# Kernel tuning notes

Measured on AMD Instinct MI355X. Metric: run time of the kernel, lower is better.

## Reference

```python
import jax, jax.numpy as jnp
import numpy as np

B, N, FREQS, DATA_DIM, WIDTH = 8192, 256, 9, 28, 128
PE_DIM = FREQS * 3 * 2  # 54


def setup_inputs() -> dict:
    rng = np.random.default_rng(0)
    mask = rng.random((B, N)) < 0.5  # ragged per-ray intersection mask
    P = int(mask.sum())             # total packed samples (~1.05M)
    key = jax.random.key(0)
    ks = jax.random.split(key, 6)
    rays_d = jax.random.normal(ks[0], (B, 3), dtype=jnp.float32)
    # sorted intersection distances along each ray (cumsum of positive steps)
    steps = jax.random.uniform(ks[1], (B, N + 1), minval=0.005, maxval=0.03)
    intrs = 2.0 + jnp.cumsum(steps, axis=1)
    data = 0.1 * jax.random.normal(ks[2], (P, DATA_DIM), dtype=jnp.float32)
    in_dim = DATA_DIM + PE_DIM
    W1 = (jax.random.normal(ks[3], (WIDTH, in_dim)) / np.sqrt(in_dim)).astype(jnp.float32)
    b1 = jnp.zeros((WIDTH,), jnp.float32)
    W2 = (jax.random.normal(ks[4], (4, WIDTH)) / np.sqrt(WIDTH)).astype(jnp.float32)
    b2 = jnp.zeros((4,), jnp.float32)
    return {"rays_d": rays_d, "intrs": intrs, "intrs_mask": jnp.asarray(mask),
            "data": data, "W1": W1, "b1": b1, "W2": W2, "b2": b2}


def pos_encode(x, freqs):
    bands = 2.0 ** jnp.arange(freqs, dtype=x.dtype)          # [F]
    xb = x[:, None, :] * bands[None, :, None]                 # [P, F, 3]
    enc = jnp.concatenate([jnp.sin(xb), jnp.cos(xb)], -1)     # [P, F, 6]
    return enc.reshape(x.shape[0], -1)                        # [P, 6F]


def _forward(rays_d, intrs, data, W1, b1, W2, b2, intrs_mask):
    Bn, Np1 = intrs.shape
    Nn = Np1 - 1
    P = data.shape[0]
    # packed row-major positions of valid samples (matches masked_scatter_ order)
    idx = jnp.flatnonzero(intrs_mask, size=P)
    ray_id = idx // Nn                       # repeat_interleave(rays_d, mask.sum(1))
    dir_pe = pos_encode(rays_d[ray_id], FREQS)
    mlp_in = jnp.concatenate([data, dir_pe], axis=-1)   # [P, data_dim + 6F]
    h = jax.nn.relu(mlp_in @ W1.T + b1)
    preact = h @ W2.T + b2                   # [P, 4]
    density_m = jax.nn.relu(preact[:, 0])
    color_m = preact[:, 1:]
    # scatter packed values back to dense [B, N] ray grid
    density = jnp.zeros((Bn * Nn,), preact.dtype).at[idx].set(density_m).reshape(Bn, Nn)
    # sigma2alpha: alpha compositing along each ray
    dists = (intrs[:, 1:] - intrs[:, :-1]) * jnp.linalg.norm(rays_d, axis=-1, keepdims=True)
    alpha = 1.0 - jnp.exp(-density * dists)
    trans = jnp.cumprod(1.0 - alpha + 1e-10, axis=-1)
    cum_light = jnp.concatenate([jnp.ones((Bn, 1), alpha.dtype), trans[:, :-1]], axis=-1)
    abs_light = alpha * cum_light            # per-sample compositing weights
    # shrgb2rgb: weighted color accumulation + white background
    color = jnp.zeros((Bn * Nn, 3), preact.dtype).at[idx].set(color_m).reshape(Bn, Nn, 3)
    rgb = jax.nn.sigmoid(color)
    comp = jnp.sum(abs_light[..., None] * rgb, axis=1)
    comp = comp + (1.0 - jnp.sum(abs_light, axis=-1))[:, None]
    return comp, alpha


def reference(rays_d, intrs, intrs_mask, data, W1, b1, W2, b2):
    return _forward(rays_d, intrs, data, W1, b1, W2, b2, intrs_mask)
```

## Files before the change

### kernel.cpp

```cpp
#include <hip/hip_runtime.h>
#include <hip/hip_bf16.h>
#include <math.h>

#define FREQS 9
#define DATA_DIM 28
#define WIDTH 128
#define IN_DIM 82
#define HST2 72
#define PEST 56

typedef float f32x4 __attribute__((ext_vector_type(4)));
typedef short s16x8 __attribute__((ext_vector_type(8)));

__device__ __forceinline__ short f2bf(float f) {
    unsigned u = __builtin_bit_cast(unsigned, f);
    u += 0x7fffu + ((u >> 16) & 1u);
    return (short)(u >> 16);
}

__device__ __forceinline__ unsigned pk2(float a, float b) {
    float2 t; t.x = a; t.y = b;
    __hip_bfloat162 h = __float22bfloat162_rn(t);
    unsigned r;
    __builtin_memcpy(&r, &h, sizeof(r));
    return r;
}

__device__ __forceinline__ float bf2f(unsigned u16v) {
    unsigned u = u16v << 16;
    return __builtin_bit_cast(float, u);
}

__device__ __forceinline__ void gload_lds16(const void* g, void* l) {
    __builtin_amdgcn_global_load_lds(
        (const __attribute__((address_space(1))) unsigned int*)g,
        (__attribute__((address_space(3))) unsigned int*)l, 16, 0, 0);
}

__device__ __forceinline__ int detect_bytemask(const unsigned* __restrict__ mw, int lane) {
    unsigned w = mw[lane & 63];
    unsigned long long hi = __ballot((w & 0xFFFFFF00u) != 0);
    return hi != 0ull;
}


__global__ __launch_bounds__(256) void k_prep(
    const float* __restrict__ rays_d, const float* __restrict__ W1,
    const float* __restrict__ b1, const float* __restrict__ W2,
    const void* __restrict__ maskp,
    short* __restrict__ W1bf, short* __restrict__ W2bf, float* __restrict__ hpe,
    int* __restrict__ cnt, int Bn, int N)
{
    int tid = threadIdx.x;
    int wid = tid >> 6, lane = tid & 63;

    if (blockIdx.x >= 256) {
        int b = (blockIdx.x - 256) * 4 + wid;
        if (b >= Bn) return;
        const unsigned char* m8 = (const unsigned char*)maskp;
        const int* m32 = (const int*)maskp;
        int fl = detect_bytemask((const unsigned*)maskp, lane);
        int base = 0;
        for (int t = 0; t < N / 64; ++t) {
            int n = t * 64 + lane;
            int mv = fl ? (int)m8[(size_t)b * N + n] : m32[(size_t)b * N + n];
            unsigned long long bal = __ballot(mv != 0);
            base += __popcll(bal);
        }
        if (lane == 0) cnt[b] = base;
        return;
    }

    __shared__ __align__(16) float w1pe[WIDTH * PEST];
    __shared__ __align__(16) float pe_s[4][PEST];

    if (blockIdx.x == 0) {
        for (int t = tid; t < WIDTH * 32; t += 256) {
            int n = t / 32, k = t - n * 32;
            W1bf[t] = (k < DATA_DIM) ? f2bf(W1[n * IN_DIM + k]) : (short)0;
        }
        for (int t = tid; t < 5 * WIDTH; t += 256) {
            int r = t >> 7, k = t & 127;
            W2bf[t] = (r < 4) ? f2bf(W2[r * WIDTH + k]) : (short)0;
        }
    }
    for (int t = tid; t < WIDTH * PEST; t += 256) {
        int row = t / PEST, j = t - row * PEST;
        w1pe[t] = (j < 54) ? W1[row * IN_DIM + DATA_DIM + j] : 0.0f;
    }
    if (lane >= 54 && lane < PEST) pe_s[wid][lane] = 0.0f;
    __syncthreads();

    int raysPer = (Bn + 255) / 256;
    for (int it = 0; it < raysPer; it += 4) {
        int b = blockIdx.x * raysPer + it + wid;
        if (b >= Bn) break;
        float dx = rays_d[b * 3 + 0], dy = rays_d[b * 3 + 1], dz = rays_d[b * 3 + 2];
        int idx = (lane < 54) ? lane : 0;
        int fb = idx / 6, t5 = idx - fb * 6;
        int ax = (t5 < 3) ? t5 : (t5 - 3);
        float dv = (ax == 0) ? dx : ((ax == 1) ? dy : dz);
        float ang = dv * (float)(1 << fb);
        float pev = (t5 < 3) ? sinf(ang) : cosf(ang);
        if (lane < 54) pe_s[wid][lane] = pev;

        #pragma unroll
        for (int rr = 0; rr < 2; ++rr) {
            int row = lane + 64 * rr;
            f32x4 s = {0.f, 0.f, 0.f, 0.f};
            #pragma unroll
            for (int j = 0; j < PEST; j += 4) {
                f32x4 wv = *reinterpret_cast<const f32x4*>(&w1pe[row * PEST + j]);
                f32x4 pv = *reinterpret_cast<const f32x4*>(&pe_s[wid][j]);
                s += wv * pv;
            }
            hpe[(size_t)b * WIDTH + row] = b1[row] + (s[0] + s[1]) + (s[2] + s[3]);
        }
    }
}

__global__ void k_scan(const int* __restrict__ cnt, int* __restrict__ roff, int Bn) {
    __shared__ int wtot[16];
    int tid = threadIdx.x;
    int lane = tid & 63, w = tid >> 6;
    int per = Bn / 1024;
    int loc[8];
    int s = 0;
    for (int i = 0; i < per; ++i) { loc[i] = s; s += cnt[tid * per + i]; }
    int inc = s;
    #pragma unroll
    for (int d = 1; d < 64; d <<= 1) {
        int o = __shfl_up(inc, d, 64);
        if (lane >= d) inc += o;
    }
    if (lane == 63) wtot[w] = inc;
    __syncthreads();
    int woff = 0;
    for (int j = 0; j < w; ++j) woff += wtot[j];
    int excl = woff + inc - s;
    for (int i = 0; i < per; ++i) roff[tid * per + i] = excl + loc[i];
}

__global__ __launch_bounds__(256) void k_packid(
    const void* __restrict__ maskp, const int* __restrict__ roff,
    unsigned* __restrict__ packid, float* __restrict__ out_alpha, int N)
{
    int wid = threadIdx.x >> 6;
    int lane = threadIdx.x & 63;
    int b = blockIdx.x * 4 + wid;
    const unsigned char* m8 = (const unsigned char*)maskp;
    const int* m32 = (const int*)maskp;
    int fl = detect_bytemask((const unsigned*)maskp, lane);
    int base = roff[b];
    for (int t = 0; t < N / 64; ++t) {
        int n = t * 64 + lane;
        int mv = fl ? (int)m8[(size_t)b * N + n] : m32[(size_t)b * N + n];
        bool m = (mv != 0);
        unsigned long long bal = __ballot(m);
        int rank = __popcll(bal & ((1ull << lane) - 1ull));
        if (m) packid[base + rank] = ((unsigned)b << 16) | (unsigned)n;
        else   out_alpha[(size_t)b * N + n] = 0.0f;
        base += __popcll(bal);
    }
}

__global__ __launch_bounds__(256, 4) void k_mlp(
    const float* __restrict__ data, const short* __restrict__ W1bf,
    const short* __restrict__ W2bf, const float* __restrict__ hpe,
    const unsigned* __restrict__ packid, uint2* __restrict__ preact, int P)
{
    int tid = threadIdx.x;
    int wid = tid >> 6;
    int lane = tid & 63;
    int g = lane >> 4, c = lane & 15;

    int nwg = gridDim.x;
    int bid = blockIdx.x;
    if (nwg >= 8) {
        int q = nwg / 8, r = nwg % 8;
        int xcd = bid % 8, off = bid / 8;
        bid = (xcd < r ? xcd * (q + 1) : r * (q + 1) + (xcd - r) * q) + off;
    }
    int q0 = bid * 256 + wid * 64;

    __shared__ __align__(16) short stageH[4][64 * HST2];

    short* hb = &stageH[wid][0];
    size_t maxoff = (size_t)P * 112 - 16;

    #pragma unroll
    for (int ci = 0; ci < 7; ++ci) {
        size_t off = (size_t)q0 * 112 + (size_t)ci * 1024 + (size_t)lane * 16;
        if (off > maxoff) off = maxoff;
        gload_lds16((const char*)data + off, (char*)hb + ci * 1024);
    }

    unsigned bs[4];
    #pragma unroll
    for (int mb = 0; mb < 4; ++mb) {
        int s = q0 + 16 * mb + c;
        s = (s < P) ? s : (P - 1);
        bs[mb] = packid[s] >> 16;
    }

    asm volatile("s_waitcnt vmcnt(0)" ::: "memory");

    const float* hbf = reinterpret_cast<const float*>(hb);
    s16x8 a0[4];
    #pragma unroll
    for (int mb = 0; mb < 4; ++mb) {
        int row = 16 * mb + c;
        unsigned u0, u1, u2, u3;
        if (g < 3) {
            f32x4 lo = *reinterpret_cast<const f32x4*>(hbf + row * 28 + 8 * g);
            f32x4 hi = *reinterpret_cast<const f32x4*>(hbf + row * 28 + 8 * g + 4);
            u0 = pk2(lo[0], lo[1]); u1 = pk2(lo[2], lo[3]);
            u2 = pk2(hi[0], hi[1]); u3 = pk2(hi[2], hi[3]);
        } else {
            f32x4 lo = *reinterpret_cast<const f32x4*>(hbf + row * 28 + 24);
            u0 = pk2(lo[0], lo[1]); u1 = pk2(lo[2], lo[3]);
            u2 = 0; u3 = 0;
        }
        uint4 uu; uu.x = u0; uu.y = u1; uu.z = u2; uu.w = u3;
        a0[mb] = __builtin_bit_cast(s16x8, uu);
    }

    const s16x8* W1v = reinterpret_cast<const s16x8*>(W1bf);
    int w2row = (c < 4) ? c : 4;
    f32x4 D[4];
    #pragma unroll
    for (int t = 0; t < 4; ++t) D[t] = (f32x4){0.f, 0.f, 0.f, 0.f};

    #pragma unroll
    for (int ms = 0; ms < 2; ++ms) {
        #pragma unroll
        for (int hh = 0; hh < 4; ++hh) {
            int nt = 4 * ms + hh;
            s16x8 Bk0 = W1v[(16 * nt + c) * 4 + g];

            f32x4 C0 = {0.f,0.f,0.f,0.f}, C1 = C0, C2 = C0, C3 = C0;
            C0 = __builtin_amdgcn_mfma_f32_16x16x32_bf16(Bk0, a0[0], C0, 0, 0, 0);
            C1 = __builtin_amdgcn_mfma_f32_16x16x32_bf16(Bk0, a0[1], C1, 0, 0, 0);
            C2 = __builtin_amdgcn_mfma_f32_16x16x32_bf16(Bk0, a0[2], C2, 0, 0, 0);
            C3 = __builtin_amdgcn_mfma_f32_16x16x32_bf16(Bk0, a0[3], C3, 0, 0, 0);

            f32x4 Cm[4] = {C0, C1, C2, C3};
            #pragma unroll
            for (int mb = 0; mb < 4; ++mb) {
                f32x4 hv = *reinterpret_cast<const f32x4*>(
                    hpe + (size_t)bs[mb] * WIDTH + 16 * nt + 4 * g);
                uint2 w;
                w.x = pk2(fmaxf(Cm[mb][0] + hv[0], 0.f), fmaxf(Cm[mb][1] + hv[1], 0.f));
                w.y = pk2(fmaxf(Cm[mb][2] + hv[2], 0.f), fmaxf(Cm[mb][3] + hv[3], 0.f));
                *reinterpret_cast<uint2*>(&hb[(16 * mb + c) * HST2 + 16 * hh + 4 * g]) = w;
            }
        }
        #pragma unroll
        for (int ks2 = 0; ks2 < 2; ++ks2) {
            s16x8 w2f = *reinterpret_cast<const s16x8*>(
                W2bf + w2row * WIDTH + 32 * (2 * ms + ks2) + 8 * g);
            #pragma unroll
            for (int t = 0; t < 4; ++t) {
                s16x8 Bf = *reinterpret_cast<const s16x8*>(
                    &hb[(16 * t + c) * HST2 + 32 * ks2 + 8 * g]);
                D[t] = __builtin_amdgcn_mfma_f32_16x16x32_bf16(w2f, Bf, D[t], 0, 0, 0);
            }
        }
    }

    if (g == 0) {
        #pragma unroll
        for (int t = 0; t < 4; ++t) {
            int s = q0 + 16 * t + c;
            if (s < P) {
                uint2 w;
                w.x = pk2(D[t][0], D[t][1]);
                w.y = pk2(D[t][2], D[t][3]);
                preact[s] = w;
            }
        }
    }
}

__global__ __launch_bounds__(256) void k_comp(
    const float* __restrict__ rays_d, const float* __restrict__ intrs,
    const uint2* __restrict__ preact, const unsigned* __restrict__ packid,
    const int* __restrict__ cnt, const int* __restrict__ roff,
    const float* __restrict__ b2, float* __restrict__ out, int Bn, int N)
{
    int wid = threadIdx.x >> 6;
    int lane = threadIdx.x & 63;
    int b = blockIdx.x * 4 + wid;

    float* out_comp = out;
    float* out_alpha = out + (size_t)Bn * 3;

    int count = cnt[b];
    int poff = roff[b];

    float dx = rays_d[b * 3 + 0], dy = rays_d[b * 3 + 1], dz = rays_d[b * 3 + 2];
    float nrm = sqrtf(dx * dx + dy * dy + dz * dz);
    f32x4 b2v = *reinterpret_cast<const f32x4*>(b2);

    float T = 1.0f;
    float aR = 0.f, aG = 0.f, aB = 0.f, aA = 0.f;

    for (int r0 = 0; r0 < count; r0 += 64) {
        int r = r0 + lane;
        bool act = (r < count);
        int ri = poff + (act ? r : 0);
        uint2 pv = preact[ri];
        unsigned pos = packid[ri];
        int n = (int)(pos & 0xffffu);

        float p0 = bf2f(pv.x & 0xffffu) + b2v[0];
        float p1 = bf2f(pv.x >> 16)     + b2v[1];
        float p2 = bf2f(pv.y & 0xffffu) + b2v[2];
        float p3 = bf2f(pv.y >> 16)     + b2v[3];

        float density = fmaxf(p0, 0.0f);
        float dist = (intrs[(size_t)b * (N + 1) + n + 1] - intrs[(size_t)b * (N + 1) + n]) * nrm;
        float alpha = act ? (1.0f - expf(-density * dist)) : 0.0f;

        float fct = 1.0f - alpha + 1e-10f;
        float scan = fct;
        #pragma unroll
        for (int d = 1; d < 64; d <<= 1) {
            float o = __shfl_up(scan, d, 64);
            if (lane >= d) scan *= o;
        }
        float tot  = __shfl(scan, 63, 64);
        float excl = __shfl_up(scan, 1, 64);
        if (lane == 0) excl = 1.0f;

        float cum  = T * excl;
        float absl = alpha * cum;
        float sR = 1.0f / (1.0f + expf(-p1));
        float sG = 1.0f / (1.0f + expf(-p2));
        float sB = 1.0f / (1.0f + expf(-p3));
        aR = fmaf(absl, sR, aR);
        aG = fmaf(absl, sG, aG);
        aB = fmaf(absl, sB, aB);
        aA += absl;
        T *= tot;

        if (act) out_alpha[(size_t)b * N + n] = alpha;
    }

    #pragma unroll
    for (int d = 32; d > 0; d >>= 1) {
        aR += __shfl_down(aR, d, 64);
        aG += __shfl_down(aG, d, 64);
        aB += __shfl_down(aB, d, 64);
        aA += __shfl_down(aA, d, 64);
    }
    if (lane == 0) {
        out_comp[b * 3 + 0] = aR + (1.0f - aA);
        out_comp[b * 3 + 1] = aG + (1.0f - aA);
        out_comp[b * 3 + 2] = aB + (1.0f - aA);
    }
}

extern "C" void kernel_launch(void* const* d_in, const int* in_sizes, int n_in,
                              void* d_out, int out_size, void* d_ws, size_t ws_size,
                              hipStream_t stream) {
    const float* rays_d = (const float*)d_in[0];
    const float* intrs  = (const float*)d_in[1];
    const void*  maskp  = d_in[2];
    const float* data   = (const float*)d_in[3];
    const float* W1     = (const float*)d_in[4];
    const float* b1     = (const float*)d_in[5];
    const float* W2     = (const float*)d_in[6];
    const float* b2     = (const float*)d_in[7];
    float* out = (float*)d_out;

    int B = in_sizes[0] / 3;
    int N = in_sizes[2] / B;
    int P = in_sizes[3] / DATA_DIM;

    int* wsI    = (int*)d_ws;
    int* cnt    = wsI + 64;
    int* roff   = wsI + 64 + B;
    short* W1bf = (short*)(wsI + 64 + 2 * B);
    short* W2bf = W1bf + WIDTH * 32;
    float* hpe  = (float*)(W2bf + 1024);
    unsigned* packid = (unsigned*)(hpe + (size_t)B * WIDTH);
    uint2* preact = (uint2*)(packid + ((P + 63) & ~63));

    float* out_alpha = out + (size_t)B * 3;

    k_prep<<<256 + B / 4, 256, 0, stream>>>(rays_d, W1, b1, W2, maskp,
                                            W1bf, W2bf, hpe, cnt, B, N);
    k_scan<<<1, 1024, 0, stream>>>(cnt, roff, B);
    k_packid<<<B / 4, 256, 0, stream>>>(maskp, roff, packid, out_alpha, N);
    k_mlp<<<(P + 255) / 256, 256, 0, stream>>>(data, W1bf, W2bf, hpe, packid, preact, P);
    k_comp<<<B / 4, 256, 0, stream>>>(rays_d, intrs, preact, packid, cnt, roff, b2,
                                      out, B, N);
}
```

Measured before the change: 89.09 us.

## Process two 64-sample tiles per wave in k_mlp with prefetched second tile

Each wave in k_mlp now handles 128 samples instead of 64, using 128-thread blocks. Both 64-row data tiles are issued as async global-to-LDS loads up front, and the wave waits only on the first (vmcnt(7)) before computing. The second tile's load then overlaps the first tile's MFMA work. The cost is fewer waves per block, an extra LDS buffer, and different occupancy bounds, which may reduce latency hiding across waves.

```diff
diff --git a/kernel.cpp b/kernel.cpp
--- a/kernel.cpp
+++ b/kernel.cpp
@@ -164,7 +164,7 @@
     }
 }
 
-__global__ __launch_bounds__(256, 4) void k_mlp(
+__global__ __launch_bounds__(128, 3) void k_mlp(
     const float* __restrict__ data, const short* __restrict__ W1bf,
     const short* __restrict__ W2bf, const float* __restrict__ hpe,
     const unsigned* __restrict__ packid, uint2* __restrict__ preact, int P)
@@ -181,102 +181,127 @@
         int xcd = bid % 8, off = bid / 8;
         bid = (xcd < r ? xcd * (q + 1) : r * (q + 1) + (xcd - r) * q) + off;
     }
-    int q0 = bid * 256 + wid * 64;
-
-    __shared__ __align__(16) short stageH[4][64 * HST2];
-
-    short* hb = &stageH[wid][0];
+    int q0 = bid * 256 + wid * 128;
+
+    __shared__ __align__(16) short regA[2][64 * HST2];
+    __shared__ __align__(16) short regB[2][3584];
+
     size_t maxoff = (size_t)P * 112 - 16;
+
+    unsigned bs0[4], bs1[4];
+    #pragma unroll
+    for (int mb = 0; mb < 4; ++mb) {
+        int s = q0 + 16 * mb + c;
+        s = (s < P) ? s : (P - 1);
+        bs0[mb] = packid[s] >> 16;
+        int s2 = q0 + 64 + 16 * mb + c;
+        s2 = (s2 < P) ? s2 : (P - 1);
+        bs1[mb] = packid[s2] >> 16;
+    }
+    __builtin_amdgcn_sched_barrier(0);
 
     #pragma unroll
     for (int ci = 0; ci < 7; ++ci) {
         size_t off = (size_t)q0 * 112 + (size_t)ci * 1024 + (size_t)lane * 16;
         if (off > maxoff) off = maxoff;
-        gload_lds16((const char*)data + off, (char*)hb + ci * 1024);
-    }
-
-    unsigned bs[4];
-    #pragma unroll
-    for (int mb = 0; mb < 4; ++mb) {
-        int s = q0 + 16 * mb + c;
-        s = (s < P) ? s : (P - 1);
-        bs[mb] = packid[s] >> 16;
-    }
-
-    asm volatile("s_waitcnt vmcnt(0)" ::: "memory");
-
-    const float* hbf = reinterpret_cast<const float*>(hb);
-    s16x8 a0[4];
-    #pragma unroll
-    for (int mb = 0; mb < 4; ++mb) {
-        int row = 16 * mb + c;
-        unsigned u0, u1, u2, u3;
-        if (g < 3) {
-            f32x4 lo = *reinterpret_cast<const f32x4*>(hbf + row * 28 + 8 * g);
-            f32x4 hi = *reinterpret_cast<const f32x4*>(hbf + row * 28 + 8 * g + 4);
-            u0 = pk2(lo[0], lo[1]); u1 = pk2(lo[2], lo[3]);
-            u2 = pk2(hi[0], hi[1]); u3 = pk2(hi[2], hi[3]);
-        } else {
-            f32x4 lo = *reinterpret_cast<const f32x4*>(hbf + row * 28 + 24);
-            u0 = pk2(lo[0], lo[1]); u1 = pk2(lo[2], lo[3]);
-            u2 = 0; u3 = 0;
-        }
-        uint4 uu; uu.x = u0; uu.y = u1; uu.z = u2; uu.w = u3;
-        a0[mb] = __builtin_bit_cast(s16x8, uu);
-    }
+        gload_lds16((const char*)data + off, (char*)&regA[wid][0] + ci * 1024);
+    }
+    __builtin_amdgcn_sched_barrier(0);
+
+    #pragma unroll
+    for (int ci = 0; ci < 7; ++ci) {
+        size_t off = (size_t)(q0 + 64) * 112 + (size_t)ci * 1024 + (size_t)lane * 16;
+        if (off > maxoff) off = maxoff;
+        gload_lds16((const char*)data + off, (char*)&regB[wid][0] + ci * 1024);
+    }
+    __builtin_amdgcn_sched_barrier(0);
+
+    asm volatile("s_waitcnt vmcnt(7)" ::: "memory");
 
     const s16x8* W1v = reinterpret_cast<const s16x8*>(W1bf);
     int w2row = (c < 4) ? c : 4;
-    f32x4 D[4];
-    #pragma unroll
-    for (int t = 0; t < 4; ++t) D[t] = (f32x4){0.f, 0.f, 0.f, 0.f};
-
-    #pragma unroll
-    for (int ms = 0; ms < 2; ++ms) {
+    short* hs = &regA[wid][0];
+
+    #pragma unroll
+    for (int bt = 0; bt < 2; ++bt) {
+        int qb = q0 + 64 * bt;
+        const unsigned* bs = bt ? bs1 : bs0;
+
+        if (bt == 1)
+            asm volatile("s_waitcnt vmcnt(0)" ::: "memory");
+
+        const float* hbf = bt ? reinterpret_cast<const float*>(&regB[wid][0])
+                              : reinterpret_cast<const float*>(&regA[wid][0]);
+        s16x8 a0[4];
         #pragma unroll
-        for (int hh = 0; hh < 4; ++hh) {
-            int nt = 4 * ms + hh;
-            s16x8 Bk0 = W1v[(16 * nt + c) * 4 + g];
-
-            f32x4 C0 = {0.f,0.f,0.f,0.f}, C1 = C0, C2 = C0, C3 = C0;
-            C0 = __builtin_amdgcn_mfma_f32_16x16x32_bf16(Bk0, a0[0], C0, 0, 0, 0);
-            C1 = __builtin_amdgcn_mfma_f32_16x16x32_bf16(Bk0, a0[1], C1, 0, 0, 0);
-            C2 = __builtin_amdgcn_mfma_f32_16x16x32_bf16(Bk0, a0[2], C2, 0, 0, 0);
-            C3 = __builtin_amdgcn_mfma_f32_16x16x32_bf16(Bk0, a0[3], C3, 0, 0, 0);
-
-            f32x4 Cm[4] = {C0, C1, C2, C3};
+        for (int mb = 0; mb < 4; ++mb) {
+            int row = 16 * mb + c;
+            unsigned u0, u1, u2, u3;
+            if (g < 3) {
+                f32x4 lo = *reinterpret_cast<const f32x4*>(hbf + row * 28 + 8 * g);
+                f32x4 hi = *reinterpret_cast<const f32x4*>(hbf + row * 28 + 8 * g + 4);
+                u0 = pk2(lo[0], lo[1]); u1 = pk2(lo[2], lo[3]);
+                u2 = pk2(hi[0], hi[1]); u3 = pk2(hi[2], hi[3]);
+            } else {
+                f32x4 lo = *reinterpret_cast<const f32x4*>(hbf + row * 28 + 24);
+                u0 = pk2(lo[0], lo[1]); u1 = pk2(lo[2], lo[3]);
+                u2 = 0; u3 = 0;
+            }
+            uint4 uu; uu.x = u0; uu.y = u1; uu.z = u2; uu.w = u3;
+            a0[mb] = __builtin_bit_cast(s16x8, uu);
+        }
+
+        f32x4 D[4];
+        #pragma unroll
+        for (int t = 0; t < 4; ++t) D[t] = (f32x4){0.f, 0.f, 0.f, 0.f};
+
+        #pragma unroll
+        for (int ms = 0; ms < 2; ++ms) {
             #pragma unroll
-            for (int mb = 0; mb < 4; ++mb) {
-                f32x4 hv = *reinterpret_cast<const f32x4*>(
-                    hpe + (size_t)bs[mb] * WIDTH + 16 * nt + 4 * g);
-                uint2 w;
-                w.x = pk2(fmaxf(Cm[mb][0] + hv[0], 0.f), fmaxf(Cm[mb][1] + hv[1], 0.f));
-                w.y = pk2(fmaxf(Cm[mb][2] + hv[2], 0.f), fmaxf(Cm[mb][3] + hv[3], 0.f));
-                *reinterpret_cast<uint2*>(&hb[(16 * mb + c) * HST2 + 16 * hh + 4 * g]) = w;
+            for (int hh = 0; hh < 4; ++hh) {
+                int nt = 4 * ms + hh;
+                s16x8 Bk0 = W1v[(16 * nt + c) * 4 + g];
+
+                f32x4 C0 = {0.f,0.f,0.f,0.f}, C1 = C0, C2 = C0, C3 = C0;
+                C0 = __builtin_amdgcn_mfma_f32_16x16x32_bf16(Bk0, a0[0], C0, 0, 0, 0);
+                C1 = __builtin_amdgcn_mfma_f32_16x16x32_bf16(Bk0, a0[1], C1, 0, 0, 0);
+                C2 = __builtin_amdgcn_mfma_f32_16x16x32_bf16(Bk0, a0[2], C2, 0, 0, 0);
+                C3 = __builtin_amdgcn_mfma_f32_16x16x32_bf16(Bk0, a0[3], C3, 0, 0, 0);
+
+                f32x4 Cm[4] = {C0, C1, C2, C3};
+                #pragma unroll
+                for (int mb = 0; mb < 4; ++mb) {
+                    f32x4 hv = *reinterpret_cast<const f32x4*>(
+                        hpe + (size_t)bs[mb] * WIDTH + 16 * nt + 4 * g);
+                    uint2 w;
+                    w.x = pk2(fmaxf(Cm[mb][0] + hv[0], 0.f), fmaxf(Cm[mb][1] + hv[1], 0.f));
+                    w.y = pk2(fmaxf(Cm[mb][2] + hv[2], 0.f), fmaxf(Cm[mb][3] + hv[3], 0.f));
+                    *reinterpret_cast<uint2*>(&hs[(16 * mb + c) * HST2 + 16 * hh + 4 * g]) = w;
+                }
             }
-        }
-        #pragma unroll
-        for (int ks2 = 0; ks2 < 2; ++ks2) {
-            s16x8 w2f = *reinterpret_cast<const s16x8*>(
-                W2bf + w2row * WIDTH + 32 * (2 * ms + ks2) + 8 * g);
+            #pragma unroll
+            for (int ks2 = 0; ks2 < 2; ++ks2) {
+                s16x8 w2f = *reinterpret_cast<const s16x8*>(
+                    W2bf + w2row * WIDTH + 32 * (2 * ms + ks2) + 8 * g);
+                #pragma unroll
+                for (int t = 0; t < 4; ++t) {
+                    s16x8 Bf = *reinterpret_cast<const s16x8*>(
+                        &hs[(16 * t + c) * HST2 + 32 * ks2 + 8 * g]);
+                    D[t] = __builtin_amdgcn_mfma_f32_16x16x32_bf16(w2f, Bf, D[t], 0, 0, 0);
+                }
+            }
+        }
+
+        if (g == 0) {
             #pragma unroll
             for (int t = 0; t < 4; ++t) {
-                s16x8 Bf = *reinterpret_cast<const s16x8*>(
-                    &hb[(16 * t + c) * HST2 + 32 * ks2 + 8 * g]);
-                D[t] = __builtin_amdgcn_mfma_f32_16x16x32_bf16(w2f, Bf, D[t], 0, 0, 0);
-            }
-        }
-    }
-
-    if (g == 0) {
-        #pragma unroll
-        for (int t = 0; t < 4; ++t) {
-            int s = q0 + 16 * t + c;
-            if (s < P) {
-                uint2 w;
-                w.x = pk2(D[t][0], D[t][1]);
-                w.y = pk2(D[t][2], D[t][3]);
-                preact[s] = w;
+                int s = qb + 16 * t + c;
+                if (s < P) {
+                    uint2 w;
+                    w.x = pk2(D[t][0], D[t][1]);
+                    w.y = pk2(D[t][2], D[t][3]);
+                    preact[s] = w;
+                }
             }
         }
     }
@@ -393,7 +418,7 @@
                                             W1bf, W2bf, hpe, cnt, B, N);
     k_scan<<<1, 1024, 0, stream>>>(cnt, roff, B);
     k_packid<<<B / 4, 256, 0, stream>>>(maskp, roff, packid, out_alpha, N);
-    k_mlp<<<(P + 255) / 256, 256, 0, stream>>>(data, W1bf, W2bf, hpe, packid, preact, P);
+    k_mlp<<<(P + 255) / 256, 128, 0, stream>>>(data, W1bf, W2bf, hpe, packid, preact, P);
     k_comp<<<B / 4, 256, 0, stream>>>(rays_d, intrs, preact, packid, cnt, roff, b2,
                                       out, B, N);
 }
```

Measured after the change: 100.0 us. 12.3% more time.
